# Kernel optimization log

Hardware: AMD Instinct MI355X
Metric: run time of the kernel (lower is better)

The kernel has to match this reference:

```python
import jax, jax.numpy as jnp
import numpy as np


def setup_inputs() -> dict:
    key = jax.random.key(0)
    k1, k2, k3, k4, k5 = jax.random.split(key, 5)
    B, S, H, K = 64, 2048, 512, 1024  # batch, src_len, hidden, key_size=2*hidden
    return {
        "query": jax.random.normal(k1, (B, 1, H), dtype=jnp.float32),
        "proj_key": jax.random.normal(k2, (B, S, H), dtype=jnp.float32),
        "encoder_hidden": jax.random.normal(k3, (B, S, K), dtype=jnp.float32),
        "mask": jnp.ones((B, 1, S), dtype=jnp.int32),
        "W_q": jax.random.normal(k4, (H, H), dtype=jnp.float32) * (1.0 / np.sqrt(H)),
        "v_energy": jax.random.normal(k5, (H,), dtype=jnp.float32) * (1.0 / np.sqrt(H)),
    }


def reference(query, proj_key, encoder_hidden, mask, W_q, v_energy):
    # query_layer: [B,1,H] @ W_q^T -> [B,1,H]
    q = jnp.einsum("bqe,he->bqh", query, W_q)
    # energy_layer(tanh(q + proj_key)): broadcast add over S, dot with v -> [B,S]
    scores = jnp.einsum("bsh,h->bs", jnp.tanh(q + proj_key), v_energy)
    scores = scores[:, None, :]  # [B,1,S]  (squeeze(2).unsqueeze(1))
    scores = jnp.where(mask == 0, -jnp.inf, scores)
    alphas = jax.nn.softmax(scores, axis=-1)  # [B,1,S]
    context = jnp.einsum("bqs,bsk->bqk", alphas, encoder_hidden)  # [B,1,K]
    return context, alphas
```

## Files before the change

### kernel.cpp

```cpp
#include <hip/hip_runtime.h>
#include <math.h>

#define BB 64
#define SS 2048
#define HH 512
#define KK 1024

__device__ __forceinline__ float fast_tanh(float x) {
    float e = __expf(2.0f * x);
    return 1.0f - 2.0f / (e + 1.0f);
}

__global__ __launch_bounds__(256) void qproj_kernel(
        const float* __restrict__ query,
        const float* __restrict__ Wq,
        float* __restrict__ q_out) {
    int wave = threadIdx.x >> 6;
    int lane = threadIdx.x & 63;
    int o = blockIdx.x * 4 + wave;
    int b = o >> 9;
    int h = o & (HH - 1);
    const float4* wrow = (const float4*)(Wq + (size_t)h * HH);
    const float4* qrow = (const float4*)(query + (size_t)b * HH);
    float4 w0 = wrow[lane * 2 + 0];
    float4 w1 = wrow[lane * 2 + 1];
    float4 x0 = qrow[lane * 2 + 0];
    float4 x1 = qrow[lane * 2 + 1];
    float acc = w0.x * x0.x + w0.y * x0.y + w0.z * x0.z + w0.w * x0.w
              + w1.x * x1.x + w1.y * x1.y + w1.z * x1.z + w1.w * x1.w;
    #pragma unroll
    for (int off = 32; off > 0; off >>= 1)
        acc += __shfl_down(acc, off, 64);
    if (lane == 0) q_out[o] = acc;
}

__global__ __launch_bounds__(256) void score_kernel(
        const float* __restrict__ pk,
        const float* __restrict__ q,
        const float* __restrict__ v,
        float* __restrict__ scores) {
    int wave = threadIdx.x >> 6;
    int lane = threadIdx.x & 63;
    int r = blockIdx.x * 4 + wave;
    int b = r >> 11;
    const float4* prow = (const float4*)(pk + (size_t)r * HH);
    const float4* qrow = (const float4*)(q + (size_t)b * HH);
    const float4* vrow = (const float4*)v;
    float acc = 0.0f;
    #pragma unroll
    for (int i = 0; i < 2; ++i) {
        float4 p = prow[lane * 2 + i];
        float4 qq = qrow[lane * 2 + i];
        float4 vv = vrow[lane * 2 + i];
        acc += fast_tanh(qq.x + p.x) * vv.x;
        acc += fast_tanh(qq.y + p.y) * vv.y;
        acc += fast_tanh(qq.z + p.z) * vv.z;
        acc += fast_tanh(qq.w + p.w) * vv.w;
    }
    #pragma unroll
    for (int off = 32; off > 0; off >>= 1)
        acc += __shfl_down(acc, off, 64);
    if (lane == 0) scores[r] = acc;
}

__global__ __launch_bounds__(256) void softmax_kernel(
        float* __restrict__ alphas,
        const int* __restrict__ mask) {
    int b = blockIdx.x;
    int t = threadIdx.x;
    float* row = alphas + (size_t)b * SS;
    const int* mrow = mask + (size_t)b * SS;
    int base = t * 8;

    float4 s0 = *(const float4*)(row + base);
    float4 s1 = *(const float4*)(row + base + 4);
    int4  m0 = *(const int4*)(mrow + base);
    int4  m1 = *(const int4*)(mrow + base + 4);
    float v[8];
    v[0] = m0.x ? s0.x : -INFINITY;
    v[1] = m0.y ? s0.y : -INFINITY;
    v[2] = m0.z ? s0.z : -INFINITY;
    v[3] = m0.w ? s0.w : -INFINITY;
    v[4] = m1.x ? s1.x : -INFINITY;
    v[5] = m1.y ? s1.y : -INFINITY;
    v[6] = m1.z ? s1.z : -INFINITY;
    v[7] = m1.w ? s1.w : -INFINITY;

    __shared__ float redmax[4];
    __shared__ float redsum[4];
    __shared__ float smax, ssum;

    float mx = v[0];
    #pragma unroll
    for (int i = 1; i < 8; ++i) mx = fmaxf(mx, v[i]);
    #pragma unroll
    for (int off = 32; off > 0; off >>= 1)
        mx = fmaxf(mx, __shfl_xor(mx, off, 64));
    if ((t & 63) == 0) redmax[t >> 6] = mx;
    __syncthreads();
    if (t == 0) smax = fmaxf(fmaxf(redmax[0], redmax[1]), fmaxf(redmax[2], redmax[3]));
    __syncthreads();
    mx = smax;

    float e[8];
    float sum = 0.0f;
    #pragma unroll
    for (int i = 0; i < 8; ++i) { e[i] = __expf(v[i] - mx); sum += e[i]; }
    #pragma unroll
    for (int off = 32; off > 0; off >>= 1)
        sum += __shfl_xor(sum, off, 64);
    if ((t & 63) == 0) redsum[t >> 6] = sum;
    __syncthreads();
    if (t == 0) ssum = redsum[0] + redsum[1] + redsum[2] + redsum[3];
    __syncthreads();
    float inv = 1.0f / ssum;

    float4 o0 = make_float4(e[0] * inv, e[1] * inv, e[2] * inv, e[3] * inv);
    float4 o1 = make_float4(e[4] * inv, e[5] * inv, e[6] * inv, e[7] * inv);
    *(float4*)(row + base)     = o0;
    *(float4*)(row + base + 4) = o1;
}

__global__ __launch_bounds__(256) void zero_kernel(float* __restrict__ p, int n) {
    int i = blockIdx.x * 256 + threadIdx.x;
    if (i < n) p[i] = 0.0f;
}

#define SCHUNK 128
__global__ __launch_bounds__(256) void context_kernel(
        const float* __restrict__ eh,
        const float* __restrict__ alphas,
        float* __restrict__ ctx) {
    int chunk = blockIdx.x;
    int b = blockIdx.y;
    int t = threadIdx.x;
    __shared__ float a_sm[SCHUNK];
    if (t < SCHUNK) a_sm[t] = alphas[(size_t)b * SS + chunk * SCHUNK + t];
    __syncthreads();
    const float4* base = (const float4*)(eh + ((size_t)b * SS + (size_t)chunk * SCHUNK) * KK);
    float4 acc = make_float4(0.f, 0.f, 0.f, 0.f);
    #pragma unroll 4
    for (int s = 0; s < SCHUNK; ++s) {
        float a = a_sm[s];
        float4 x = base[(size_t)s * (KK / 4) + t];
        acc.x += a * x.x;
        acc.y += a * x.y;
        acc.z += a * x.z;
        acc.w += a * x.w;
    }
    float* c = ctx + (size_t)b * KK + t * 4;
    atomicAdd(c + 0, acc.x);
    atomicAdd(c + 1, acc.y);
    atomicAdd(c + 2, acc.z);
    atomicAdd(c + 3, acc.w);
}

extern "C" void kernel_launch(void* const* d_in, const int* in_sizes, int n_in,
                              void* d_out, int out_size, void* d_ws, size_t ws_size,
                              hipStream_t stream) {
    const float* query    = (const float*)d_in[0];
    const float* proj_key = (const float*)d_in[1];
    const float* eh       = (const float*)d_in[2];
    const int*   mask     = (const int*)  d_in[3];
    const float* Wq       = (const float*)d_in[4];
    const float* venergy  = (const float*)d_in[5];

    float* ctx    = (float*)d_out;
    float* alphas = (float*)d_out + BB * KK;

    float* q_tmp = ctx;

    qproj_kernel<<<(BB * HH) / 4, 256, 0, stream>>>(query, Wq, q_tmp);

    score_kernel<<<(BB * SS) / 4, 256, 0, stream>>>(proj_key, q_tmp, venergy, alphas);

    softmax_kernel<<<BB, 256, 0, stream>>>(alphas, mask);

    zero_kernel<<<(BB * KK) / 256, 256, 0, stream>>>(ctx, BB * KK);

    context_kernel<<<dim3(SS / SCHUNK, BB), 256, 0, stream>>>(eh, alphas, ctx);
}
```

Baseline: 826.2 us.

## Replace atomic context accumulation with workspace partials and add two-rows-per-wave scoring

When a large enough workspace is available, the context kernel writes per-chunk partial sums to the workspace and a separate reduce kernel sums them. This replaces the zero-fill kernel and the float atomics on the output. The query projection and score kernels now have each wave compute two output rows, reusing the q and v loads and halving the grid. The cost is an extra 4 MB partial buffer that must be written and read back, and the partial path runs only if the harness provides the workspace.

Result: no change. 830.9 us (+0.6%).

```diff
diff --git a/kernel.cpp b/kernel.cpp
--- a/kernel.cpp
+++ b/kernel.cpp
@@ -5,6 +5,8 @@
 #define SS 2048
 #define HH 512
 #define KK 1024
+#define SCHUNK 128
+#define NCHUNK (SS / SCHUNK)
 
 __device__ __forceinline__ float fast_tanh(float x) {
     float e = __expf(2.0f * x);
@@ -17,21 +19,30 @@
         float* __restrict__ q_out) {
     int wave = threadIdx.x >> 6;
     int lane = threadIdx.x & 63;
-    int o = blockIdx.x * 4 + wave;
-    int b = o >> 9;
-    int h = o & (HH - 1);
-    const float4* wrow = (const float4*)(Wq + (size_t)h * HH);
-    const float4* qrow = (const float4*)(query + (size_t)b * HH);
-    float4 w0 = wrow[lane * 2 + 0];
-    float4 w1 = wrow[lane * 2 + 1];
-    float4 x0 = qrow[lane * 2 + 0];
-    float4 x1 = qrow[lane * 2 + 1];
-    float acc = w0.x * x0.x + w0.y * x0.y + w0.z * x0.z + w0.w * x0.w
-              + w1.x * x1.x + w1.y * x1.y + w1.z * x1.z + w1.w * x1.w;
-    #pragma unroll
-    for (int off = 32; off > 0; off >>= 1)
-        acc += __shfl_down(acc, off, 64);
-    if (lane == 0) q_out[o] = acc;
+    int o0 = (blockIdx.x * 4 + wave) * 2;
+    int b = o0 >> 9;
+    int h0 = o0 & (HH - 1);
+    const float4* w0r = (const float4*)(Wq + (size_t)h0 * HH);
+    const float4* w1r = (const float4*)(Wq + (size_t)(h0 + 1) * HH);
+    const float4* qr  = (const float4*)(query + (size_t)b * HH);
+    float a0 = 0.0f, a1 = 0.0f;
+    #pragma unroll
+    for (int i = 0; i < 2; ++i) {
+        float4 x  = qr[lane * 2 + i];
+        float4 wa = w0r[lane * 2 + i];
+        float4 wb = w1r[lane * 2 + i];
+        a0 += wa.x * x.x + wa.y * x.y + wa.z * x.z + wa.w * x.w;
+        a1 += wb.x * x.x + wb.y * x.y + wb.z * x.z + wb.w * x.w;
+    }
+    #pragma unroll
+    for (int off = 32; off > 0; off >>= 1) {
+        a0 += __shfl_down(a0, off, 64);
+        a1 += __shfl_down(a1, off, 64);
+    }
+    if (lane == 0) {
+        q_out[o0]     = a0;
+        q_out[o0 + 1] = a1;
+    }
 }
 
 __global__ __launch_bounds__(256) void score_kernel(
@@ -41,26 +52,37 @@
         float* __restrict__ scores) {
     int wave = threadIdx.x >> 6;
     int lane = threadIdx.x & 63;
-    int r = blockIdx.x * 4 + wave;
-    int b = r >> 11;
-    const float4* prow = (const float4*)(pk + (size_t)r * HH);
-    const float4* qrow = (const float4*)(q + (size_t)b * HH);
-    const float4* vrow = (const float4*)v;
-    float acc = 0.0f;
+    int r0 = (blockIdx.x * 4 + wave) * 2;
+    int b = r0 >> 11;
+    const float4* p0r = (const float4*)(pk + (size_t)r0 * HH);
+    const float4* p1r = (const float4*)(pk + (size_t)(r0 + 1) * HH);
+    const float4* qr  = (const float4*)(q + (size_t)b * HH);
+    const float4* vr  = (const float4*)v;
+    float a0 = 0.0f, a1 = 0.0f;
     #pragma unroll
     for (int i = 0; i < 2; ++i) {
-        float4 p = prow[lane * 2 + i];
-        float4 qq = qrow[lane * 2 + i];
-        float4 vv = vrow[lane * 2 + i];
-        acc += fast_tanh(qq.x + p.x) * vv.x;
-        acc += fast_tanh(qq.y + p.y) * vv.y;
-        acc += fast_tanh(qq.z + p.z) * vv.z;
-        acc += fast_tanh(qq.w + p.w) * vv.w;
-    }
-    #pragma unroll
-    for (int off = 32; off > 0; off >>= 1)
-        acc += __shfl_down(acc, off, 64);
-    if (lane == 0) scores[r] = acc;
+        float4 p0 = p0r[lane * 2 + i];
+        float4 p1 = p1r[lane * 2 + i];
+        float4 qq = qr[lane * 2 + i];
+        float4 vv = vr[lane * 2 + i];
+        a0 += fast_tanh(qq.x + p0.x) * vv.x;
+        a0 += fast_tanh(qq.y + p0.y) * vv.y;
+        a0 += fast_tanh(qq.z + p0.z) * vv.z;
+        a0 += fast_tanh(qq.w + p0.w) * vv.w;
+        a1 += fast_tanh(qq.x + p1.x) * vv.x;
+        a1 += fast_tanh(qq.y + p1.y) * vv.y;
+        a1 += fast_tanh(qq.z + p1.z) * vv.z;
+        a1 += fast_tanh(qq.w + p1.w) * vv.w;
+    }
+    #pragma unroll
+    for (int off = 32; off > 0; off >>= 1) {
+        a0 += __shfl_down(a0, off, 64);
+        a1 += __shfl_down(a1, off, 64);
+    }
+    if (lane == 0) {
+        scores[r0]     = a0;
+        scores[r0 + 1] = a1;
+    }
 }
 
 __global__ __launch_bounds__(256) void softmax_kernel(
@@ -121,16 +143,10 @@
     *(float4*)(row + base + 4) = o1;
 }
 
-__global__ __launch_bounds__(256) void zero_kernel(float* __restrict__ p, int n) {
-    int i = blockIdx.x * 256 + threadIdx.x;
-    if (i < n) p[i] = 0.0f;
-}
-
-#define SCHUNK 128
-__global__ __launch_bounds__(256) void context_kernel(
+__global__ __launch_bounds__(256) void context_partial_kernel(
         const float* __restrict__ eh,
         const float* __restrict__ alphas,
-        float* __restrict__ ctx) {
+        float* __restrict__ ws) {
     int chunk = blockIdx.x;
     int b = blockIdx.y;
     int t = threadIdx.x;
@@ -148,6 +164,54 @@
         acc.z += a * x.z;
         acc.w += a * x.w;
     }
+    float4* out = (float4*)(ws + (size_t)(chunk * BB + b) * KK);
+    out[t] = acc;
+}
+
+__global__ __launch_bounds__(256) void context_reduce_kernel(
+        const float* __restrict__ ws,
+        float* __restrict__ ctx) {
+    int g = blockIdx.x * 256 + threadIdx.x;
+    const float4* w = (const float4*)ws;
+    const size_t plane = (size_t)BB * KK / 4;
+    float4 acc = w[g];
+    #pragma unroll
+    for (int c = 1; c < NCHUNK; ++c) {
+        float4 x = w[(size_t)c * plane + g];
+        acc.x += x.x;
+        acc.y += x.y;
+        acc.z += x.z;
+        acc.w += x.w;
+    }
+    ((float4*)ctx)[g] = acc;
+}
+
+__global__ __launch_bounds__(256) void zero_kernel(float* __restrict__ p, int n) {
+    int i = blockIdx.x * 256 + threadIdx.x;
+    if (i < n) p[i] = 0.0f;
+}
+
+__global__ __launch_bounds__(256) void context_atomic_kernel(
+        const float* __restrict__ eh,
+        const float* __restrict__ alphas,
+        float* __restrict__ ctx) {
+    int chunk = blockIdx.x;
+    int b = blockIdx.y;
+    int t = threadIdx.x;
+    __shared__ float a_sm[SCHUNK];
+    if (t < SCHUNK) a_sm[t] = alphas[(size_t)b * SS + chunk * SCHUNK + t];
+    __syncthreads();
+    const float4* base = (const float4*)(eh + ((size_t)b * SS + (size_t)chunk * SCHUNK) * KK);
+    float4 acc = make_float4(0.f, 0.f, 0.f, 0.f);
+    #pragma unroll 4
+    for (int s = 0; s < SCHUNK; ++s) {
+        float a = a_sm[s];
+        float4 x = base[(size_t)s * (KK / 4) + t];
+        acc.x += a * x.x;
+        acc.y += a * x.y;
+        acc.z += a * x.z;
+        acc.w += a * x.w;
+    }
     float* c = ctx + (size_t)b * KK + t * 4;
     atomicAdd(c + 0, acc.x);
     atomicAdd(c + 1, acc.y);
@@ -168,15 +232,25 @@
     float* ctx    = (float*)d_out;
     float* alphas = (float*)d_out + BB * KK;
 
-    float* q_tmp = ctx;
-
-    qproj_kernel<<<(BB * HH) / 4, 256, 0, stream>>>(query, Wq, q_tmp);
-
-    score_kernel<<<(BB * SS) / 4, 256, 0, stream>>>(proj_key, q_tmp, venergy, alphas);
-
-    softmax_kernel<<<BB, 256, 0, stream>>>(alphas, mask);
-
-    zero_kernel<<<(BB * KK) / 256, 256, 0, stream>>>(ctx, BB * KK);
-
-    context_kernel<<<dim3(SS / SCHUNK, BB), 256, 0, stream>>>(eh, alphas, ctx);
-}
+    const size_t par_floats = (size_t)NCHUNK * BB * KK;
+    const size_t need_bytes = (par_floats + (size_t)BB * HH) * sizeof(float);
+
+    if (d_ws != nullptr && ws_size >= need_bytes) {
+        float* wsf    = (float*)d_ws;
+        float* ws_par = wsf;
+        float* q_tmp  = wsf + par_floats;
+
+        qproj_kernel<<<(BB * HH) / 8, 256, 0, stream>>>(query, Wq, q_tmp);
+        score_kernel<<<(BB * SS) / 8, 256, 0, stream>>>(proj_key, q_tmp, venergy, alphas);
+        softmax_kernel<<<BB, 256, 0, stream>>>(alphas, mask);
+        context_partial_kernel<<<dim3(NCHUNK, BB), 256, 0, stream>>>(eh, alphas, ws_par);
+        context_reduce_kernel<<<(BB * KK) / (256 * 4), 256, 0, stream>>>(ws_par, ctx);
+    } else {
+        float* q_tmp = ctx;
+        qproj_kernel<<<(BB * HH) / 8, 256, 0, stream>>>(query, Wq, q_tmp);
+        score_kernel<<<(BB * SS) / 8, 256, 0, stream>>>(proj_key, q_tmp, venergy, alphas);
+        softmax_kernel<<<BB, 256, 0, stream>>>(alphas, mask);
+        zero_kernel<<<(BB * KK) / 256, 256, 0, stream>>>(ctx, BB * KK);
+        context_atomic_kernel<<<dim3(NCHUNK, BB), 256, 0, stream>>>(eh, alphas, ctx);
+    }
+}
```
